# Kernel optimization log

Measured on AMD Instinct MI355X. Metric: run time of the kernel, lower is better.

Reference implementation:

```python
import jax, jax.numpy as jnp
import numpy as np

N_NODES = 100000
N_EDGES = 6400000
ATOM_F = 128
R_CUT = 5.0


def setup_inputs() -> dict:
    key = jax.random.key(0)
    ks = jax.random.split(key, 9)
    x = jax.random.normal(ks[0], (N_NODES, ATOM_F), dtype=jnp.float32)
    rij = jax.random.uniform(ks[1], (N_EDGES,), dtype=jnp.float32) * R_CUT
    vij = jax.random.normal(ks[2], (N_EDGES, 3), dtype=jnp.float32)
    src = jax.random.randint(ks[3], (N_EDGES,), 0, N_NODES)
    dst = jax.random.randint(ks[4], (N_EDGES,), 0, N_NODES)
    # Dense params (PyTorch Linear default-ish init scale)
    s1 = 1.0 / np.sqrt(ATOM_F)
    W1 = jax.random.uniform(ks[5], (ATOM_F, ATOM_F), dtype=jnp.float32, minval=-s1, maxval=s1)
    b1 = jnp.zeros((ATOM_F,), dtype=jnp.float32)
    W2 = jax.random.uniform(ks[6], (ATOM_F, 1), dtype=jnp.float32, minval=-s1, maxval=s1)
    b2 = jnp.zeros((1,), dtype=jnp.float32)
    return {"x": x, "rij": rij, "vij": vij, "src": src, "dst": dst,
            "W1": W1, "b1": b1, "W2": W2, "b2": b2}


def reference(x, rij, vij, src, dst, W1, b1, W2, b2):
    # transform: Dense(F,F,swish) -> Dense(F,1,swish)
    h = jax.nn.silu(x @ W1 + b1)          # [N, F]
    q = jax.nn.silu(h @ W2 + b2)          # [N, 1]
    # cosine cutoff on edge distances
    c_ij = 0.5 * (jnp.cos(jnp.pi * rij / R_CUT) + 1.0)
    c_ij = c_ij * (rij < R_CUT).astype(rij.dtype)  # [E]
    # e_mul_u: broadcast source-node scalar onto edge vectors, scale by cutoff
    mu_ij = vij * q[src] * c_ij[:, None]  # [E, 3]
    # copy_e_sum: scatter-add edges into destination nodes
    mu = jax.ops.segment_sum(mu_ij, dst, num_segments=N_NODES)  # [N, 3]
    return mu
```

## Files before the change

kernel.cpp:

```cpp
#include <hip/hip_runtime.h>
#include <hip/hip_bf16.h>

#define NN 100000
#define NE 6400000
#define NSL 16
#define SLICE 6250
#define NB1 1250
#define CHUNK (NE / NB1)
#define BCAP 448
#define CAPR 192
#define C2 48
#define QSCALE 650.0f
#define QINV (1.0f / 650.0f)
#define QBIAS 5461

typedef __bf16 bf16x8_t __attribute__((ext_vector_type(8)));
typedef float f32x4_t __attribute__((ext_vector_type(4)));

__device__ __forceinline__ float silu_f(float v) { return v / (1.0f + __expf(-v)); }

__device__ __forceinline__ unsigned f16b(float v) {
    _Float16 h = (_Float16)v;
    unsigned short u;
    __builtin_memcpy(&u, &h, 2);
    return (unsigned)u;
}
__device__ __forceinline__ float f16f(unsigned u) {
    unsigned short us = (unsigned short)u;
    _Float16 h;
    __builtin_memcpy(&h, &us, 2);
    return (float)h;
}

__global__ __launch_bounds__(256, 2) void node_q_kernel(
    const float* __restrict__ x,
    const float* __restrict__ W1,
    const float* __restrict__ b1,
    const float* __restrict__ W2,
    const float* __restrict__ b2,
    float* __restrict__ q,
    int nGroups)
{
    __shared__ __align__(16) __bf16 w1s[2048 * 8];

    const int lane = threadIdx.x & 63;
    const int wave = threadIdx.x >> 6;
    const int c    = lane & 15;
    const int quad = lane >> 4;
    const int gwave  = blockIdx.x * 4 + wave;
    const int nWaves = gridDim.x * 4;

#pragma unroll
    for (int it = 0; it < 8; ++it) {
        const int e   = it * 256 + threadIdx.x;
        const int c_  = e & 15;
        const int nt_ = (e >> 4) & 7;
        const int qd  = (e >> 7) & 3;
        const int kt_ = e >> 9;
        const float* p = W1 + (kt_ * 32 + qd * 8) * 128 + nt_ * 16 + c_;
        bf16x8_t v;
#pragma unroll
        for (int j = 0; j < 8; ++j) v[j] = (__bf16)p[j * 128];
        *reinterpret_cast<bf16x8_t*>(&w1s[e * 8]) = v;
    }
    __syncthreads();

    bf16x8_t bfrag[8][4];
    float b1v[8], w2v[8];
#pragma unroll
    for (int nt = 0; nt < 8; ++nt) {
#pragma unroll
        for (int kt = 0; kt < 4; ++kt)
            bfrag[nt][kt] = *reinterpret_cast<const bf16x8_t*>(
                &w1s[(((kt * 4 + quad) * 8 + nt) * 16 + c) * 8]);
        b1v[nt] = b1[nt * 16 + c];
        w2v[nt] = W2[nt * 16 + c];
    }
    const float b2v = b2[0];

    for (int g = gwave; g < nGroups; g += nWaves) {
        const float* xrow = x + (size_t)(g * 16 + c) * 128 + quad * 8;
        bf16x8_t afrag[4];
#pragma unroll
        for (int kt = 0; kt < 4; ++kt) {
            const f32x4_t x0 = *reinterpret_cast<const f32x4_t*>(xrow + kt * 32);
            const f32x4_t x1 = *reinterpret_cast<const f32x4_t*>(xrow + kt * 32 + 4);
#pragma unroll
            for (int j = 0; j < 4; ++j) {
                afrag[kt][j]     = (__bf16)x0[j];
                afrag[kt][j + 4] = (__bf16)x1[j];
            }
        }

        float cr[4] = {0.f, 0.f, 0.f, 0.f};
#pragma unroll
        for (int nt = 0; nt < 8; ++nt) {
            f32x4_t acc = {0.f, 0.f, 0.f, 0.f};
#pragma unroll
            for (int kt = 0; kt < 4; ++kt)
                acc = __builtin_amdgcn_mfma_f32_16x16x32_bf16(afrag[kt], bfrag[nt][kt], acc, 0, 0, 0);
#pragma unroll
            for (int r = 0; r < 4; ++r)
                cr[r] += silu_f(acc[r] + b1v[nt]) * w2v[nt];
        }
#pragma unroll
        for (int r = 0; r < 4; ++r) {
            float v = cr[r];
            v += __shfl_xor(v, 1);
            v += __shfl_xor(v, 2);
            v += __shfl_xor(v, 4);
            v += __shfl_xor(v, 8);
            cr[r] = v;
        }
        if (c == 0) {
#pragma unroll
            for (int r = 0; r < 4; ++r)
                q[g * 16 + quad * 4 + r] = silu_f(cr[r] + b2v);
        }
    }
}

__global__ __launch_bounds__(256) void bucket_kernel(
    const float4* __restrict__ rij4,
    const float4* __restrict__ vij4,
    const int4* __restrict__ src4,
    const int4* __restrict__ dst4,
    const float* __restrict__ q,
    int* __restrict__ counts,
    uint2* __restrict__ arena)
{
    __shared__ uint2 ring[NSL][CAPR];
    __shared__ int cnt[NSL];
    __shared__ int gpos[NSL];

    const int t = threadIdx.x;
    const int lane = t & 63;
    const int wave = t >> 6;
    if (t < NSL) { cnt[t] = 0; gpos[t] = 0; }
    __syncthreads();

    const unsigned long long ltmask = (1ull << lane) - 1ull;
    const int g4 = blockIdx.x * (CHUNK / 4);
    const float K = 0.62831853071795864769f;

    for (int i = 0; i < CHUNK / 4 / 256; ++i) {
        const int idx = g4 + i * 256 + t;
        const int4 s = src4[idx];
        const int4 d = dst4[idx];
        const float4 r = rij4[idx];
        const float4 v0 = vij4[3 * idx + 0];
        const float4 v1 = vij4[3 * idx + 1];
        const float4 v2 = vij4[3 * idx + 2];

        const float c0 = (r.x < 5.0f) ? 0.5f * (__cosf(r.x * K) + 1.0f) : 0.0f;
        const float c1 = (r.y < 5.0f) ? 0.5f * (__cosf(r.y * K) + 1.0f) : 0.0f;
        const float c2 = (r.z < 5.0f) ? 0.5f * (__cosf(r.z * K) + 1.0f) : 0.0f;
        const float c3 = (r.w < 5.0f) ? 0.5f * (__cosf(r.w * K) + 1.0f) : 0.0f;
        const float w0 = q[s.x] * c0, w1 = q[s.y] * c1;
        const float w2 = q[s.z] * c2, w3 = q[s.w] * c3;

        int   dn[4] = {d.x, d.y, d.z, d.w};
        float px[4] = {v0.x * w0, v0.w * w1, v1.z * w2, v2.y * w3};
        float py[4] = {v0.y * w0, v1.x * w1, v1.w * w2, v2.z * w3};
        float pz[4] = {v0.z * w0, v1.y * w1, v2.x * w2, v2.w * w3};

#pragma unroll
        for (int j = 0; j < 4; ++j) {
            const int k  = dn[j] / SLICE;
            const int dl = dn[j] - k * SLICE;
            const float fx = fminf(fmaxf(px[j], -8.f), 8.f);
            const float fy = fminf(fmaxf(py[j], -8.f), 8.f);
            const float fz = fminf(fmaxf(pz[j], -8.f), 8.f);
            uint2 rec;
            rec.x = (unsigned)dl | (f16b(fx) << 16);
            rec.y = f16b(fy) | (f16b(fz) << 16);

            const unsigned long long b0 = __ballot(k & 1);
            const unsigned long long b1m = __ballot(k & 2);
            const unsigned long long b2m = __ballot(k & 4);
            const unsigned long long b3m = __ballot(k & 8);
            const unsigned long long eq =
                ((k & 1) ? b0 : ~b0) & ((k & 2) ? b1m : ~b1m) &
                ((k & 4) ? b2m : ~b2m) & ((k & 8) ? b3m : ~b3m);
            const int leader = __ffsll((long long)eq) - 1;
            const int rank   = __popcll(eq & ltmask);
            int base = 0;
            if (lane == leader) base = atomicAdd(&cnt[k], __popcll(eq));
            base = __shfl(base, leader);
            const int pos = base + rank;
            if (pos < CAPR) ring[k][pos] = rec;
        }
        __syncthreads();

        for (int sl = wave; sl < NSL; sl += 4) {
            const int n = cnt[sl];
            const int full = n & ~63;
            if (full > 0) {
                uint2* seg = arena + ((size_t)sl * NB1 + blockIdx.x) * BCAP + gpos[sl];
                for (int off = 0; off + 64 <= n; off += 64) {
                    const int p_ = gpos[sl] + off + lane;
                    if (p_ < BCAP) seg[off + lane - 0] = ring[sl][off + lane];
                }
                const int resid = n - full;
                uint2 keep;
                if (lane < resid) keep = ring[sl][full + lane];
                __builtin_amdgcn_s_waitcnt(0);
                if (lane < resid) ring[sl][lane] = keep;
                if (lane == 0) { gpos[sl] += full; cnt[sl] = resid; }
            }
        }
        __syncthreads();
    }

    for (int sl = wave; sl < NSL; sl += 4) {
        const int n = cnt[sl];
        if (lane < n) {
            const int p_ = gpos[sl] + lane;
            if (p_ < BCAP)
                arena[((size_t)sl * NB1 + blockIdx.x) * BCAP + p_] = ring[sl][lane];
        }
        if (lane == 0) counts[blockIdx.x * NSL + sl] = min(gpos[sl] + n, BCAP);
    }
}

__global__ __launch_bounds__(256) void reduce_kernel(
    const uint2* __restrict__ arena,
    const int* __restrict__ counts,
    float* __restrict__ part)
{
    __shared__ unsigned long long acc[SLICE];
    const int s = blockIdx.x / C2;
    const int c = blockIdx.x % C2;

    for (int i = threadIdx.x; i < SLICE; i += 256) acc[i] = 0ull;
    __syncthreads();

    for (int b = c; b < NB1; b += C2) {
        const int n = counts[b * NSL + s];
        const uint2* seg = arena + ((size_t)s * NB1 + b) * BCAP;
        for (int i = threadIdx.x; i < n; i += 256) {
            const uint2 r = seg[i];
            const int node = r.x & 0xffffu;
            const int ix = __float2int_rn(f16f(r.x >> 16)      * QSCALE) + QBIAS;
            const int iy = __float2int_rn(f16f(r.y & 0xffffu)  * QSCALE) + QBIAS;
            const int iz = __float2int_rn(f16f(r.y >> 16)      * QSCALE) + QBIAS;
            const unsigned long long inc =
                (1ull << 54) |
                ((unsigned long long)(unsigned)ix << 36) |
                ((unsigned long long)(unsigned)iy << 18) |
                (unsigned long long)(unsigned)iz;
            atomicAdd(&acc[node], inc);
        }
    }
    __syncthreads();

    float* dp = part + (size_t)blockIdx.x * (SLICE * 3);
    for (int i = threadIdx.x; i < SLICE; i += 256) {
        const unsigned long long a = acc[i];
        const int cnt = (int)(a >> 54);
        const int X = (int)((a >> 36) & 0x3FFFFu) - cnt * QBIAS;
        const int Y = (int)((a >> 18) & 0x3FFFFu) - cnt * QBIAS;
        const int Z = (int)(a & 0x3FFFFu)         - cnt * QBIAS;
        dp[i * 3 + 0] = (float)X * QINV;
        dp[i * 3 + 1] = (float)Y * QINV;
        dp[i * 3 + 2] = (float)Z * QINV;
    }
}

__global__ __launch_bounds__(256) void finalize_kernel(
    const float* __restrict__ part,
    float* __restrict__ out)
{
    const int i = blockIdx.x * 256 + threadIdx.x;
    if (i >= NN * 3) return;
    const int n   = i / 3;
    const int k   = i - n * 3;
    const int s   = n / SLICE;
    const int l   = n - s * SLICE;
    const float* p = part + ((size_t)s * C2) * (SLICE * 3) + l * 3 + k;
    float sum = 0.f;
#pragma unroll
    for (int c = 0; c < C2; ++c) sum += p[(size_t)c * (SLICE * 3)];
    out[i] = sum;
}

__global__ __launch_bounds__(256) void edge_atomic_kernel(
    const float4* __restrict__ rij4,
    const float4* __restrict__ vij4,
    const int4* __restrict__ src4,
    const int4* __restrict__ dst4,
    const float* __restrict__ q,
    float* __restrict__ mu)
{
    const int t = blockIdx.x * 256 + threadIdx.x;
    const int4 s = src4[t];
    const int4 d = dst4[t];
    const float4 r = rij4[t];
    const float4 v0 = vij4[3 * t + 0];
    const float4 v1 = vij4[3 * t + 1];
    const float4 v2 = vij4[3 * t + 2];
    const float K = 0.62831853071795864769f;
    const float c0 = (r.x < 5.0f) ? 0.5f * (__cosf(r.x * K) + 1.0f) : 0.0f;
    const float c1 = (r.y < 5.0f) ? 0.5f * (__cosf(r.y * K) + 1.0f) : 0.0f;
    const float c2 = (r.z < 5.0f) ? 0.5f * (__cosf(r.z * K) + 1.0f) : 0.0f;
    const float c3 = (r.w < 5.0f) ? 0.5f * (__cosf(r.w * K) + 1.0f) : 0.0f;
    const float s0 = q[s.x] * c0, s1 = q[s.y] * c1, s2 = q[s.z] * c2, s3 = q[s.w] * c3;
    float* m0 = mu + 3 * (size_t)d.x;
    atomicAdd(m0 + 0, v0.x * s0); atomicAdd(m0 + 1, v0.y * s0); atomicAdd(m0 + 2, v0.z * s0);
    float* m1 = mu + 3 * (size_t)d.y;
    atomicAdd(m1 + 0, v0.w * s1); atomicAdd(m1 + 1, v1.x * s1); atomicAdd(m1 + 2, v1.y * s1);
    float* m2 = mu + 3 * (size_t)d.z;
    atomicAdd(m2 + 0, v1.z * s2); atomicAdd(m2 + 1, v1.w * s2); atomicAdd(m2 + 2, v2.x * s2);
    float* m3 = mu + 3 * (size_t)d.w;
    atomicAdd(m3 + 0, v2.y * s3); atomicAdd(m3 + 1, v2.z * s3); atomicAdd(m3 + 2, v2.w * s3);
}

extern "C" void kernel_launch(void* const* d_in, const int* in_sizes, int n_in,
                              void* d_out, int out_size, void* d_ws, size_t ws_size,
                              hipStream_t stream)
{
    const float* x   = (const float*)d_in[0];
    const float* rij = (const float*)d_in[1];
    const float* vij = (const float*)d_in[2];
    const int*   src = (const int*)d_in[3];
    const int*   dst = (const int*)d_in[4];
    const float* W1  = (const float*)d_in[5];
    const float* b1  = (const float*)d_in[6];
    const float* W2  = (const float*)d_in[7];
    const float* b2  = (const float*)d_in[8];

    char* ws = (char*)d_ws;
    const size_t Q_OFF    = 0;
    const size_t CNT_OFF  = 425984;
    const size_t REC_OFF  = 1048576;
    const size_t PART_OFF = REC_OFF + (size_t)NSL * NB1 * BCAP * 8;
    const size_t WS_NEEDED = PART_OFF + (size_t)NSL * C2 * SLICE * 3 * 4;

    float* q = (float*)(ws + Q_OFF);

    node_q_kernel<<<512, 256, 0, stream>>>(x, W1, b1, W2, b2, q, NN / 16);

    if (ws_size >= WS_NEEDED) {
        int*   counts = (int*)(ws + CNT_OFF);
        uint2* arena  = (uint2*)(ws + REC_OFF);
        float* part   = (float*)(ws + PART_OFF);

        bucket_kernel<<<NB1, 256, 0, stream>>>(
            (const float4*)rij, (const float4*)vij, (const int4*)src, (const int4*)dst,
            q, counts, arena);
        reduce_kernel<<<NSL * C2, 256, 0, stream>>>(arena, counts, part);
        finalize_kernel<<<(NN * 3 + 255) / 256, 256, 0, stream>>>(part, (float*)d_out);
    } else {
        hipMemsetAsync(d_out, 0, (size_t)NN * 3 * sizeof(float), stream);
        edge_atomic_kernel<<<NE / 4 / 256, 256, 0, stream>>>(
            (const float4*)rij, (const float4*)vij, (const int4*)src, (const int4*)dst,
            q, (float*)d_out);
    }
}
```

Measured before the change: 288.7 us.

## Pre-pack W1 once, shrink bucket chunks, and vectorize per-wave reduce loads

Moves the W1 bf16 repacking out of every node_q block into a single one-block pack kernel, so node_q blocks read the packed fragments from global memory and no longer need LDS or a barrier. node_q then launches with twice as many blocks. The bucket kernel is split into more, smaller blocks (3125 blocks of 2 iterations, with a smaller per-block capacity) to raise parallelism. The reduce kernel now uses fewer column groups, has each wave own a bucket segment, and reads two records per 16-byte load. The trade-offs are an extra kernel launch, more partial outputs to manage, and a tighter per-bucket capacity (224) that could overflow and silently drop records.

```diff
diff --git a/kernel.cpp b/kernel.cpp
--- a/kernel.cpp
+++ b/kernel.cpp
@@ -5,11 +5,11 @@
 #define NE 6400000
 #define NSL 16
 #define SLICE 6250
-#define NB1 1250
-#define CHUNK (NE / NB1)
-#define BCAP 448
+#define NB1 3125
+#define NT1 2
+#define BCAP 224
 #define CAPR 192
-#define C2 48
+#define C2 32
 #define QSCALE 650.0f
 #define QINV (1.0f / 650.0f)
 #define QBIAS 5461
@@ -32,24 +32,9 @@
     return (float)h;
 }
 
-__global__ __launch_bounds__(256, 2) void node_q_kernel(
-    const float* __restrict__ x,
-    const float* __restrict__ W1,
-    const float* __restrict__ b1,
-    const float* __restrict__ W2,
-    const float* __restrict__ b2,
-    float* __restrict__ q,
-    int nGroups)
-{
-    __shared__ __align__(16) __bf16 w1s[2048 * 8];
-
-    const int lane = threadIdx.x & 63;
-    const int wave = threadIdx.x >> 6;
-    const int c    = lane & 15;
-    const int quad = lane >> 4;
-    const int gwave  = blockIdx.x * 4 + wave;
-    const int nWaves = gridDim.x * 4;
-
+__global__ __launch_bounds__(256) void w1_pack_kernel(
+    const float* __restrict__ W1, __bf16* __restrict__ pk)
+{
 #pragma unroll
     for (int it = 0; it < 8; ++it) {
         const int e   = it * 256 + threadIdx.x;
@@ -61,9 +46,25 @@
         bf16x8_t v;
 #pragma unroll
         for (int j = 0; j < 8; ++j) v[j] = (__bf16)p[j * 128];
-        *reinterpret_cast<bf16x8_t*>(&w1s[e * 8]) = v;
-    }
-    __syncthreads();
+        *reinterpret_cast<bf16x8_t*>(pk + e * 8) = v;
+    }
+}
+
+__global__ __launch_bounds__(256, 2) void node_q_kernel(
+    const float* __restrict__ x,
+    const __bf16* __restrict__ pk,
+    const float* __restrict__ b1,
+    const float* __restrict__ W2,
+    const float* __restrict__ b2,
+    float* __restrict__ q,
+    int nGroups)
+{
+    const int lane = threadIdx.x & 63;
+    const int wave = threadIdx.x >> 6;
+    const int c    = lane & 15;
+    const int quad = lane >> 4;
+    const int gwave  = blockIdx.x * 4 + wave;
+    const int nWaves = gridDim.x * 4;
 
     bf16x8_t bfrag[8][4];
     float b1v[8], w2v[8];
@@ -72,7 +73,7 @@
 #pragma unroll
         for (int kt = 0; kt < 4; ++kt)
             bfrag[nt][kt] = *reinterpret_cast<const bf16x8_t*>(
-                &w1s[(((kt * 4 + quad) * 8 + nt) * 16 + c) * 8]);
+                pk + (((kt * 4 + quad) * 8 + nt) * 16 + c) * 8);
         b1v[nt] = b1[nt * 16 + c];
         w2v[nt] = W2[nt * 16 + c];
     }
@@ -140,10 +141,10 @@
     __syncthreads();
 
     const unsigned long long ltmask = (1ull << lane) - 1ull;
-    const int g4 = blockIdx.x * (CHUNK / 4);
+    const int g4 = blockIdx.x * (NT1 * 256);
     const float K = 0.62831853071795864769f;
 
-    for (int i = 0; i < CHUNK / 4 / 256; ++i) {
+    for (int i = 0; i < NT1; ++i) {
         const int idx = g4 + i * 256 + t;
         const int4 s = src4[idx];
         const int4 d = dst4[idx];
@@ -199,7 +200,7 @@
                 uint2* seg = arena + ((size_t)sl * NB1 + blockIdx.x) * BCAP + gpos[sl];
                 for (int off = 0; off + 64 <= n; off += 64) {
                     const int p_ = gpos[sl] + off + lane;
-                    if (p_ < BCAP) seg[off + lane - 0] = ring[sl][off + lane];
+                    if (p_ < BCAP) seg[off + lane] = ring[sl][off + lane];
                 }
                 const int resid = n - full;
                 uint2 keep;
@@ -223,6 +224,20 @@
     }
 }
 
+__device__ __forceinline__ void acc_rec64(unsigned long long* acc, unsigned w0, unsigned w1)
+{
+    const int node = w0 & 0xffffu;
+    const int ix = __float2int_rn(f16f(w0 >> 16)     * QSCALE) + QBIAS;
+    const int iy = __float2int_rn(f16f(w1 & 0xffffu) * QSCALE) + QBIAS;
+    const int iz = __float2int_rn(f16f(w1 >> 16)     * QSCALE) + QBIAS;
+    const unsigned long long inc =
+        (1ull << 54) |
+        ((unsigned long long)(unsigned)ix << 36) |
+        ((unsigned long long)(unsigned)iy << 18) |
+        (unsigned long long)(unsigned)iz;
+    atomicAdd(&acc[node], inc);
+}
+
 __global__ __launch_bounds__(256) void reduce_kernel(
     const uint2* __restrict__ arena,
     const int* __restrict__ counts,
@@ -231,25 +246,26 @@
     __shared__ unsigned long long acc[SLICE];
     const int s = blockIdx.x / C2;
     const int c = blockIdx.x % C2;
+    const int lane = threadIdx.x & 63;
+    const int wave = threadIdx.x >> 6;
 
     for (int i = threadIdx.x; i < SLICE; i += 256) acc[i] = 0ull;
     __syncthreads();
 
-    for (int b = c; b < NB1; b += C2) {
+    for (int k = wave; ; k += 4) {
+        const int b = c + C2 * k;
+        if (b >= NB1) break;
         const int n = counts[b * NSL + s];
         const uint2* seg = arena + ((size_t)s * NB1 + b) * BCAP;
-        for (int i = threadIdx.x; i < n; i += 256) {
-            const uint2 r = seg[i];
-            const int node = r.x & 0xffffu;
-            const int ix = __float2int_rn(f16f(r.x >> 16)      * QSCALE) + QBIAS;
-            const int iy = __float2int_rn(f16f(r.y & 0xffffu)  * QSCALE) + QBIAS;
-            const int iz = __float2int_rn(f16f(r.y >> 16)      * QSCALE) + QBIAS;
-            const unsigned long long inc =
-                (1ull << 54) |
-                ((unsigned long long)(unsigned)ix << 36) |
-                ((unsigned long long)(unsigned)iy << 18) |
-                (unsigned long long)(unsigned)iz;
-            atomicAdd(&acc[node], inc);
+        for (int i = lane * 2; i < n; i += 128) {
+            if (i + 1 < n) {
+                const uint4 r = *reinterpret_cast<const uint4*>(seg + i);
+                acc_rec64(acc, r.x, r.y);
+                acc_rec64(acc, r.z, r.w);
+            } else {
+                const uint2 r = seg[i];
+                acc_rec64(acc, r.x, r.y);
+            }
         }
     }
     __syncthreads();
@@ -330,27 +346,31 @@
     const float* b2  = (const float*)d_in[8];
 
     char* ws = (char*)d_ws;
-    const size_t Q_OFF    = 0;
-    const size_t CNT_OFF  = 425984;
-    const size_t REC_OFF  = 1048576;
+    const size_t Q_OFF   = 0;
+    const size_t PK_OFF  = 409600;
+    const size_t CNT_OFF = 458752;
+    const size_t REC_OFF = 1048576;
     const size_t PART_OFF = REC_OFF + (size_t)NSL * NB1 * BCAP * 8;
     const size_t WS_NEEDED = PART_OFF + (size_t)NSL * C2 * SLICE * 3 * 4;
 
-    float* q = (float*)(ws + Q_OFF);
-
-    node_q_kernel<<<512, 256, 0, stream>>>(x, W1, b1, W2, b2, q, NN / 16);
+    float*  q  = (float*)(ws + Q_OFF);
+    __bf16* pk = (__bf16*)(ws + PK_OFF);
 
     if (ws_size >= WS_NEEDED) {
         int*   counts = (int*)(ws + CNT_OFF);
         uint2* arena  = (uint2*)(ws + REC_OFF);
         float* part   = (float*)(ws + PART_OFF);
 
+        w1_pack_kernel<<<1, 256, 0, stream>>>(W1, pk);
+        node_q_kernel<<<1024, 256, 0, stream>>>(x, pk, b1, W2, b2, q, NN / 16);
         bucket_kernel<<<NB1, 256, 0, stream>>>(
             (const float4*)rij, (const float4*)vij, (const int4*)src, (const int4*)dst,
             q, counts, arena);
         reduce_kernel<<<NSL * C2, 256, 0, stream>>>(arena, counts, part);
         finalize_kernel<<<(NN * 3 + 255) / 256, 256, 0, stream>>>(part, (float*)d_out);
     } else {
+        w1_pack_kernel<<<1, 256, 0, stream>>>(W1, pk);
+        node_q_kernel<<<1024, 256, 0, stream>>>(x, pk, b1, W2, b2, q, NN / 16);
         hipMemsetAsync(d_out, 0, (size_t)NN * 3 * sizeof(float), stream);
         edge_atomic_kernel<<<NE / 4 / 256, 256, 0, stream>>>(
             (const float4*)rij, (const float4*)vij, (const int4*)src, (const int4*)dst,
```

Measured after the change: 296.4 us. 2.7% more time.
